# Performance work log

Measured on AMD Instinct MI355X. Metric: run time of the kernel, lower is better.

Reference implementation:

```python
import jax, jax.numpy as jnp
import numpy as np

N_WIRES = 16
VAR_DEPTH = 2
BATCH = 16


def _param_sizes():
    sizes = []
    n = N_WIRES
    lay = 0
    while n > 1:
        sizes.append(4 * int(np.ceil(N_WIRES / 2 ** lay)) * VAR_DEPTH)
        n = (n + 1) // 2
        lay += 1
    return sizes  # [128, 64, 32, 16]


def _apply_1q(psi, gate, w):
    # psi: (B, 2, ..., 2); gate: (2,2) complex; wire w lives on axis w+1
    psi = jnp.moveaxis(psi, w + 1, -1)
    psi = jnp.einsum('...j,ij->...i', psi, gate)
    return jnp.moveaxis(psi, -1, w + 1)


def _rx(psi, th, w):
    c = jnp.cos(th / 2).astype(jnp.complex64)
    s = jnp.sin(th / 2).astype(jnp.complex64)
    gate = jnp.stack([jnp.stack([c, -1j * s]), jnp.stack([-1j * s, c])])
    return _apply_1q(psi, gate, w)


def _rz(psi, th, w):
    ph = jnp.exp(0.5j * th * jnp.array([-1.0, 1.0], jnp.float32)).astype(jnp.complex64)
    shape = [1] * psi.ndim
    shape[w + 1] = 2
    return psi * ph.reshape(shape)


def _rzz(psi, th, wa, wb):
    # diag(e^{-i t/2}, e^{i t/2}, e^{i t/2}, e^{-i t/2}) -> sign = -1 if bits equal else +1
    sgn = jnp.array([[-1.0, 1.0], [1.0, -1.0]], jnp.float32)
    ph = jnp.exp(0.5j * th * sgn).astype(jnp.complex64)  # symmetric, transpose-safe
    a, b = min(wa, wb) + 1, max(wa, wb) + 1
    shape = [1] * psi.ndim
    shape[a] = 2
    shape[b] = 2
    return psi * ph.reshape(shape)


def _cnot(psi, c, t):
    p0 = jax.lax.slice_in_dim(psi, 0, 1, axis=c + 1)
    p1 = jax.lax.slice_in_dim(psi, 1, 2, axis=c + 1)
    return jnp.concatenate([p0, jnp.flip(p1, axis=t + 1)], axis=c + 1)


def _conv_layer(psi, params, active):
    n = len(active)
    for d in range(VAR_DEPTH):
        for j in range(n):
            base = 4 * j + d * 4 * n
            psi = _rx(psi, params[base + 0], active[j])
            psi = _rz(psi, params[base + 1], active[j])
            psi = _rx(psi, params[base + 2], active[j])
        for bg in (0, 1):
            for j in range(bg, n, 2):
                jn = (j + 1) % n  # ring coupling (wraps last->first)
                base = 4 * j + d * 4 * n
                psi = _rzz(psi, params[base + 3], active[j], active[jn])
    return psi


def _pool(psi, active):
    for j in range(0, len(active), 2):
        if j + 1 < len(active):
            psi = _cnot(psi, active[j], active[j + 1])
    return psi, active[::2]


def _forward(psi, params_list):
    active = list(range(N_WIRES))
    for p in params_list:
        psi = _conv_layer(psi, p, active)
        if len(active) > 1:
            psi, active = _pool(psi, active)
    w = active[0]  # measure Z on the surviving wire (wire 0)
    prob = psi.real ** 2 + psi.imag ** 2
    axes = tuple(a for a in range(1, psi.ndim) if a != w + 1)
    p2 = prob.sum(axis=axes)  # (B, 2)
    return p2[:, 0] - p2[:, 1]


def setup_inputs() -> dict:
    key = jax.random.key(0)
    ks = jax.random.split(key, 8)
    dim = 2 ** N_WIRES
    x_re = jax.random.normal(ks[0], (BATCH, dim), dtype=jnp.float32)
    x_im = jax.random.normal(ks[1], (BATCH, dim), dtype=jnp.float32)
    nrm = jnp.sqrt(jnp.sum(x_re ** 2 + x_im ** 2, axis=1, keepdims=True))
    x_re = x_re / nrm
    x_im = x_im / nrm
    sizes = _param_sizes()
    two_pi = 2.0 * np.pi
    params = [jax.random.uniform(ks[2 + i], (sizes[i],), dtype=jnp.float32) * two_pi
              for i in range(len(sizes))]
    return {"x_re": x_re, "x_im": x_im,
            "params0": params[0], "params1": params[1],
            "params2": params[2], "params3": params[3]}


def reference(x_re, x_im, params0, params1, params2, params3):
    psi = (x_re + 1j * x_im).astype(jnp.complex64)
    psi = psi.reshape((BATCH,) + (2,) * N_WIRES)
    return _forward(psi, [params0, params1, params2, params3])
```

## Files before the change

### kernel.cpp

```cpp
#include <hip/hip_runtime.h>


#define DEV __device__ __forceinline__

__device__ static const unsigned char G_CP[60] = {
  15,14,13,12,11,10,9,8,7,6,5,4,3,2,1,0,
  15,14,13,12,11,10,9,8,7,6,5,4,3,2,1,0,
  15,13,11,9,7,5,3,1,
  15,13,11,9,7,5,3,1,
  15,11,7,3,
  15,11,7,3,
  15,7,
  15,7
};
__device__ static const unsigned char G_CQ[60] = {
  14,13,12,11,10,9,8,7,6,5,4,3,2,1,0,15,
  14,13,12,11,10,9,8,7,6,5,4,3,2,1,0,15,
  13,11,9,7,5,3,1,15,
  13,11,9,7,5,3,1,15,
  11,7,3,15,
  11,7,3,15,
  7,15,
  7,15
};

DEV float2 F2(float x, float y){ float2 r; r.x = x; r.y = y; return r; }
DEV float2 cmulf(float2 a, float2 b){ return F2(a.x*b.x - a.y*b.y, a.x*b.y + a.y*b.x); }
DEV int swz(int j){ return j ^ ((j>>4)&15) ^ ((j>>8)&15); }
DEV int sw2(int m){
  return m ^ ((m>>9)&1) ^ (((m>>11)&1)<<1)
           ^ ((((m>>3)&1)^((m>>8)&1))<<2)
           ^ ((((m>>4)&1)^((m>>5)&1)^((m>>10)&1))<<3);
}

#if __has_builtin(__builtin_amdgcn_permlane32_swap)
#define HAVE_PLS 1
DEV void plswap01(float &x0, float &x1){
  auto r = __builtin_amdgcn_permlane32_swap(__float_as_uint(x0), __float_as_uint(x1), false, false);
  x0 = __uint_as_float((unsigned)r[0]);
  x1 = __uint_as_float((unsigned)r[1]);
}
#else
#define HAVE_PLS 0
#endif

template<int SB>
DEV void gate4(float2* a, const float* __restrict__ g){
  const float4 lo = *(const float4*)g;
  const float4 hi = *(const float4*)(g + 4);
  float u00r=lo.x,u00i=lo.y,u01r=lo.z,u01i=lo.w;
  float u11r=hi.x,u11i=hi.y,u10r=hi.z,u10i=hi.w;
  #pragma unroll
  for (int m=0;m<2;m++){
    int i0 = (SB==0) ? (m<<1) : m;
    int i1 = i0 | (1<<SB);
    float2 x0=a[i0], x1=a[i1];
    a[i0] = F2(u00r*x0.x - u00i*x0.y + u01r*x1.x - u01i*x1.y,
               u00r*x0.y + u00i*x0.x + u01r*x1.y + u01i*x1.x);
    a[i1] = F2(u10r*x0.x - u10i*x0.y + u11r*x1.x - u11i*x1.y,
               u10r*x0.y + u10i*x0.x + u11r*x1.y + u11i*x1.x);
  }
}

DEV void lgate(float2* a, const float* __restrict__ g, int mask, int lane){
  const float4 cf = *(const float4*)(g + ((lane & mask) ? 4 : 0));
  float Ar=cf.x, Ai=cf.y, Br=cf.z, Bi=cf.w;
  #pragma unroll
  for (int s=0;s<4;s++){
    float px = __shfl_xor(a[s].x, mask);
    float py = __shfl_xor(a[s].y, mask);
    a[s] = F2(Ar*a[s].x - Ai*a[s].y + Br*px - Bi*py,
              Ar*a[s].y + Ai*a[s].x + Br*py + Bi*px);
  }
}

DEV void lgate32(float2* a, const float* __restrict__ g, int lane){
#if HAVE_PLS
  bool h = (lane & 32) != 0;
  const float4 cf = *(const float4*)(g + (h ? 4 : 0));
  float c0r = h ? cf.z : cf.x, c0i = h ? cf.w : cf.y;
  float c1r = h ? cf.x : cf.z, c1i = h ? cf.y : cf.w;
  #pragma unroll
  for (int s=0;s<4;s++){
    float x0x = a[s].x, x1x = a[s].x, x0y = a[s].y, x1y = a[s].y;
    plswap01(x0x, x1x); plswap01(x0y, x1y);
    a[s] = F2(c0r*x0x - c0i*x0y + c1r*x1x - c1i*x1y,
              c0r*x0y + c0i*x0x + c1r*x1y + c1i*x1x);
  }
#else
  lgate(a, g, 32, lane);
#endif
}

DEV void cswap(float2* a, int cmask, int tmask, int lane){
  bool c = (lane & cmask) != 0;
  #pragma unroll
  for (int s=0;s<4;s++){
    float px = __shfl_xor(a[s].x, tmask);
    float py = __shfl_xor(a[s].y, tmask);
    if (c){ a[s].x = px; a[s].y = py; }
  }
}

template<int C0,int N0,int C1,int N1,unsigned M0,unsigned M1>
DEV void diagv(float2* a, const float* __restrict__ hh, const float* __restrict__ cs, unsigned Ib){
  const unsigned rm = M0|M1;
  float b0 = 0.f, b1 = 0.f;
  #pragma unroll
  for (int k=C0;k<C0+N0;k++){
    const int p=G_CP[k], q=G_CQ[k];
    if (!(((1u<<p)|(1u<<q)) & rm)){
      float h = hh[k];
      float v = (((Ib>>p)^(Ib>>q))&1u) ? h : -h;
      if (k & 1) b1 += v; else b0 += v;
    }
  }
  #pragma unroll
  for (int k=C1;k<C1+N1;k++){
    const int p=G_CP[k], q=G_CQ[k];
    if (!(((1u<<p)|(1u<<q)) & rm)){
      float h = hh[k];
      float v = (((Ib>>p)^(Ib>>q))&1u) ? h : -h;
      if (k & 1) b1 += v; else b0 += v;
    }
  }
  float cb, sb;
  __sincosf(b0 + b1, &sb, &cb);
  #pragma unroll
  for (int r=0;r<4;r++){
    unsigned Ir = Ib ^ ((r&1)?M0:0u) ^ ((r&2)?M1:0u);
    float Fr = cb, Fi = sb;
    #pragma unroll
    for (int k=C0;k<C0+N0;k++){
      const int p=G_CP[k], q=G_CQ[k];
      if (((1u<<p)|(1u<<q)) & rm){
        float ck = cs[2*k], sk = cs[2*k+1];
        float ss = (((Ir>>p)^(Ir>>q))&1u) ? sk : -sk;
        float nr = Fr*ck - Fi*ss, ni = Fr*ss + Fi*ck;
        Fr = nr; Fi = ni;
      }
    }
    #pragma unroll
    for (int k=C1;k<C1+N1;k++){
      const int p=G_CP[k], q=G_CQ[k];
      if (((1u<<p)|(1u<<q)) & rm){
        float ck = cs[2*k], sk = cs[2*k+1];
        float ss = (((Ir>>p)^(Ir>>q))&1u) ? sk : -sk;
        float nr = Fr*ck - Fi*ss, ni = Fr*ss + Fi*ck;
        Fr = nr; Fi = ni;
      }
    }
    a[r] = cmulf(a[r], F2(Fr, Fi));
  }
}

DEV void build_entry(float* sh, const float* __restrict__ p0, const float* __restrict__ p1,
                     const float* __restrict__ p2, const float* __restrict__ p3, int g){
  int d, j, n; const float* P;
  if (g < 32)      { n=16; d=(g>>4)&1; j=g&15; P=p0; }
  else if (g < 48) { n=8;  d=(g>>3)&1; j=g&7;  P=p1; }
  else if (g < 56) { n=4;  d=(g>>2)&1; j=g&3;  P=p2; }
  else             { n=2;  d=(g>>1)&1; j=g&1;  P=p3; }
  int base = 4*j + 4*n*d;
  float th0 = P[base+0], th1 = P[base+1], th2 = P[base+2], th3 = P[base+3];
  float c0,s0,ca,sa,c2,s2;
  sincosf(0.5f*th0, &s0, &c0);
  sincosf(0.5f*th1, &sa, &ca);
  sincosf(0.5f*th2, &s2, &c2);
  float B00r =  ca*c0, B00i = -sa*c0;
  float B01r = -sa*s0, B01i = -ca*s0;
  float B10r =  sa*s0, B10i = -ca*s0;
  float B11r =  ca*c0, B11i =  sa*c0;
  float* o8 = sh + g*8;
  o8[0]=c2*B00r + s2*B10i; o8[1]=c2*B00i - s2*B10r;
  o8[2]=c2*B01r + s2*B11i; o8[3]=c2*B01i - s2*B11r;
  o8[4]=s2*B01i + c2*B11r; o8[5]=-s2*B01r + c2*B11i;
  o8[6]=s2*B00i + c2*B10r; o8[7]=-s2*B00r + c2*B10i;
  sh[480 + g] = 0.5f*th3;
  float ch, shn;
  sincosf(0.5f*th3, &shn, &ch);
  sh[544 + 2*g]     = ch;
  sh[544 + 2*g + 1] = shn;
}

__global__ __launch_bounds__(1024, 4)
void k_pa(const float* __restrict__ xre, const float* __restrict__ xim,
          const float* __restrict__ pp0, const float* __restrict__ pp1,
          const float* __restrict__ pp2, const float* __restrict__ pp3,
          float* __restrict__ tbl, float2* __restrict__ st, float* __restrict__ out){
  const int t = threadIdx.x, lane = t & 63, wv = t >> 6;
  const int batch = blockIdx.x >> 4, o = blockIdx.x & 15;
  const unsigned hi = ((unsigned)batch<<16) | ((unsigned)o<<12);
  __shared__ float2 lds[4096];
  __shared__ float sh[672];
  float2 a[4];
  {
    unsigned base = hi | ((unsigned)t<<2);
    float4 re = *(const float4*)(xre + base);
    float4 im = *(const float4*)(xim + base);
    a[0]=F2(re.x,im.x); a[1]=F2(re.y,im.y); a[2]=F2(re.z,im.z); a[3]=F2(re.w,im.w);
  }
  if (t < 60) build_entry(sh, pp0, pp1, pp2, pp3, t);
  if (blockIdx.x == 0 && t >= 64 && t < 80) out[t - 64] = 0.f;
  __syncthreads();
  if (blockIdx.x == 0){
    for (int i = t; i < 664; i += 1024) tbl[i] = sh[i];
  }
  #define LTB(i) (sh + (i)*8)
  const float* HH = sh + 480;
  const float* CS = sh + 544;
  gate4<0>(a, LTB(15)); gate4<1>(a, LTB(14));
  lgate(a, LTB(13),1,lane); lgate(a, LTB(12),2,lane);
  lgate(a, LTB(11),4,lane); lgate(a, LTB(10),8,lane);
  lgate(a, LTB(9),16,lane); lgate32(a, LTB(8),lane);
  const unsigned IbA = ((unsigned)o<<12) | ((unsigned)wv<<8) | ((unsigned)lane<<2);
  diagv<8,7,0,0,1u,2u>(a, HH, CS, IbA);
  gate4<1>(a, LTB(30));
  lgate(a, LTB(29),1,lane); lgate(a, LTB(28),2,lane);
  lgate(a, LTB(27),4,lane); lgate(a, LTB(26),8,lane);
  lgate(a, LTB(25),16,lane);
  diagv<25,5,0,0,1u,2u>(a, HH, CS, IbA);
  cswap(a,2,1,lane);
  cswap(a,8,4,lane);
  #pragma unroll
  for (int s=0;s<4;s++) lds[swz((t<<2)|s)] = a[s];
  __syncthreads();
  const int idxR = (wv&15) | (((lane>>4)&1)<<4) | (((lane>>5)&1)<<5)
                 | (((lane>>2)&1)<<6) | (((lane>>3)&1)<<7)
                 | ((lane&1)<<8) | (((lane>>1)&1)<<9);
  #pragma unroll
  for (int s=0;s<4;s++) a[s] = lds[swz(idxR | ((s&1)<<10) | (((s>>1)&1)<<11))];
  lgate(a, LTB(7),1,lane); lgate(a, LTB(6),2,lane);
  gate4<0>(a, LTB(5)); gate4<1>(a, LTB(4));
  const unsigned IbB = ((unsigned)o<<12) | (unsigned)idxR;
  diagv<4,4,0,0,1024u,2048u>(a, HH, CS, IbB);
  lgate(a, LTB(24),8,lane);
  lgate(a, LTB(23),1,lane); lgate(a, LTB(22),2,lane);
  gate4<0>(a, LTB(21));
  diagv<21,4,0,0,1024u,2048u>(a, HH, CS, IbB);
  cswap(a,8,4,lane);
  cswap(a,2,1,lane);
  {
    unsigned sb = hi | ((unsigned)wv<<8) | ((unsigned)lane<<2);
    float4 v0, v1;
    v0.x=a[0].x; v0.y=a[0].y; v0.z=a[1].x; v0.w=a[1].y;
    v1.x=a[2].x; v1.y=a[2].y; v1.z=a[3].x; v1.w=a[3].y;
    *(float4*)(st + sb) = v0;
    *(float4*)(st + sb + 2) = v1;
  }
  #undef LTB
}

__global__ __launch_bounds__(1024, 4)
void k_pb(const float* __restrict__ tbl, float2* __restrict__ st, float* __restrict__ out){
  const int t = threadIdx.x, lane = t & 63, wv = t >> 6;
  const int batch = blockIdx.x >> 4, o = blockIdx.x & 15;
  __shared__ float2 lds[4096];
  __shared__ float shB[672];
  __shared__ float red[16];
  const unsigned opart = ((unsigned)(o&1)<<2) | ((unsigned)((o>>1)&1)<<4)
                       | ((unsigned)((o>>2)&1)<<6) | ((unsigned)((o>>3)&1)<<8);
  float2 a[4];
  {
    unsigned gb = ((unsigned)batch<<16)
      | (((unsigned)(o>>3)&1)<<2) | (((unsigned)(o>>2)&1)<<4)
      | (((unsigned)(o>>1)&1)<<6) | (((unsigned)o&1)<<10)
      | (((unsigned)(wv>>3)&1)<<3) | (((unsigned)(wv>>2)&1)<<5)
      | (((unsigned)(wv>>1)&1)<<7) | (((unsigned)wv&1)<<11)
      | (((unsigned)(lane>>4)&1)<<8) | (((unsigned)(lane>>5)&1)<<9)
      | (((unsigned)lane&1)<<12) | (((unsigned)(lane>>1)&1)<<13)
      | (((unsigned)(lane>>2)&1)<<14) | (((unsigned)(lane>>3)&1)<<15);
    const float4* sp = (const float4*)(st + gb);
    float4 lo = sp[0], hi4 = sp[1];
    if (t < 664) shB[t] = tbl[t];
    a[0]=F2(lo.x,lo.y); a[1]=F2(lo.z,lo.w); a[2]=F2(hi4.x,hi4.y); a[3]=F2(hi4.z,hi4.w);
  }
  __syncthreads();
  #define TBL(i) (shB + (i)*8)
  const float* HH = shB + 480;
  const float* CS = shB + 544;
  const unsigned IbA = opart
    | (((unsigned)lane&1)<<12) | (((unsigned)(lane>>1)&1)<<13)
    | (((unsigned)(lane>>2)&1)<<14) | (((unsigned)(lane>>3)&1)<<15)
    | (((unsigned)(lane>>4)&1)<<0) | (((unsigned)(lane>>5)&1)<<1)
    | (((unsigned)wv&1)<<3) | (((unsigned)(wv>>1)&1)<<5)
    | (((unsigned)(wv>>2)&1)<<7) | (((unsigned)(wv>>3)&1)<<9);
  lgate(a, TBL(3),1,lane); lgate(a, TBL(2),2,lane);
  lgate(a, TBL(1),4,lane); lgate(a, TBL(0),8,lane);
  diagv<0,4,15,1,1024u,2048u>(a, HH, CS, IbA);
  lgate(a, TBL(31),16,lane);
  gate4<1>(a, TBL(20));
  lgate(a, TBL(19),1,lane); lgate(a, TBL(18),2,lane);
  lgate(a, TBL(17),4,lane); lgate(a, TBL(16),8,lane);
  diagv<16,5,30,2,1024u,2048u>(a, HH, CS, IbA);
  cswap(a,8,4,lane);
  cswap(a,2,1,lane);
  cswap(a,32,16,lane);
  { float2 tmp=a[2]; a[2]=a[3]; a[3]=tmp; }
  const int idxW = ((lane>>4)&1) | (((lane>>5)&1)<<1)
                 | ((wv&1)<<2) | (((wv>>1)&1)<<3) | (((wv>>2)&1)<<4) | (((wv>>3)&1)<<5)
                 | ((lane&1)<<8) | (((lane>>1)&1)<<9)
                 | (((lane>>2)&1)<<10) | (((lane>>3)&1)<<11);
  #pragma unroll
  for (int s=0;s<4;s++) lds[sw2(idxW | ((s&1)<<6) | (((s>>1)&1)<<7))] = a[s];
  __syncthreads();
  const int idxR = (wv&1) | (((wv>>1)&1)<<6) | (((wv>>2)&1)<<8) | (((wv>>3)&1)<<10)
                 | ((lane&1)<<3) | (((lane>>1)&1)<<4) | (((lane>>2)&1)<<5)
                 | (((lane>>3)&1)<<7) | (((lane>>4)&1)<<9) | (((lane>>5)&1)<<11);
  #pragma unroll
  for (int s=0;s<4;s++) a[s] = lds[sw2(idxR | ((s&1)<<1) | (((s>>1)&1)<<2))];
  const unsigned IbB = opart
    | (((unsigned)wv&1)<<0) | (((unsigned)(wv>>1)&1)<<10)
    | (((unsigned)(wv>>2)&1)<<12) | (((unsigned)(wv>>3)&1)<<14)
    | (((unsigned)lane&1)<<5) | (((unsigned)(lane>>1)&1)<<7)
    | (((unsigned)(lane>>2)&1)<<9) | (((unsigned)(lane>>3)&1)<<11)
    | (((unsigned)(lane>>4)&1)<<13) | (((unsigned)(lane>>5)&1)<<15);
  gate4<0>(a, TBL(39)); gate4<1>(a, TBL(38));
  lgate(a, TBL(37),1,lane); lgate(a, TBL(36),2,lane); lgate(a, TBL(35),4,lane);
  lgate(a, TBL(34),8,lane); lgate(a, TBL(33),16,lane); lgate32(a, TBL(32),lane);
  diagv<32,8,0,0,2u,8u>(a, HH, CS, IbB);
  gate4<0>(a, TBL(47)); gate4<1>(a, TBL(46));
  lgate(a, TBL(45),1,lane); lgate(a, TBL(44),2,lane); lgate(a, TBL(43),4,lane);
  lgate(a, TBL(42),8,lane); lgate(a, TBL(41),16,lane); lgate32(a, TBL(40),lane);
  diagv<40,8,0,0,2u,8u>(a, HH, CS, IbB);
  cswap(a,32,16,lane); cswap(a,8,4,lane); cswap(a,2,1,lane);
  { float2 tmp=a[2]; a[2]=a[3]; a[3]=tmp; }
  lgate32(a, TBL(48),lane); lgate(a, TBL(49),8,lane); lgate(a, TBL(50),2,lane);
  gate4<1>(a, TBL(51));
  diagv<48,4,0,0,2u,8u>(a, HH, CS, IbB);
  lgate32(a, TBL(52),lane); lgate(a, TBL(53),8,lane); lgate(a, TBL(54),2,lane);
  gate4<1>(a, TBL(55));
  diagv<52,4,0,0,2u,8u>(a, HH, CS, IbB);
  cswap(a,32,8,lane);
  if (lane & 2){
    float2 t0=a[0]; a[0]=a[2]; a[2]=t0;
    float2 t1=a[1]; a[1]=a[3]; a[3]=t1;
  }
  lgate32(a, TBL(56),lane); lgate(a, TBL(57),2,lane);
  diagv<56,2,0,0,2u,8u>(a, HH, CS, IbB);
  lgate32(a, TBL(58),lane);
  float sl = 0.f;
  #pragma unroll
  for (int s=0;s<4;s++) sl += a[s].x*a[s].x + a[s].y*a[s].y;
  float sg = (lane & 32) ? -sl : sl;
  #pragma unroll
  for (int off=32; off>0; off>>=1) sg += __shfl_down(sg, off);
  if ((t & 63) == 0) red[wv] = sg;
  __syncthreads();
  if (t == 0){
    float tot = 0.f;
    #pragma unroll
    for (int w=0; w<16; w++) tot += red[w];
    atomicAdd(out + batch, tot);
  }
  #undef TBL
}

extern "C" void kernel_launch(void* const* d_in, const int* in_sizes, int n_in,
                              void* d_out, int out_size, void* d_ws, size_t ws_size,
                              hipStream_t stream) {
  const float* xre = (const float*)d_in[0];
  const float* xim = (const float*)d_in[1];
  const float* p0  = (const float*)d_in[2];
  const float* p1  = (const float*)d_in[3];
  const float* p2  = (const float*)d_in[4];
  const float* p3  = (const float*)d_in[5];
  float* out = (float*)d_out;
  float2* st = (float2*)d_ws;
  float* tbl = (float*)((char*)d_ws + (8u<<20));

  k_pa<<<256, 1024, 0, stream>>>(xre, xim, p0, p1, p2, p3, tbl, st, out);
  k_pb<<<256, 1024, 0, stream>>>(tbl, st, out);
}
```

Baseline: 106.2 us.

## Fuse two kernels into one cooperative kernel with a grid-wide sync

```diff
diff --git a/kernel.cpp b/kernel.cpp
--- a/kernel.cpp
+++ b/kernel.cpp
@@ -1,4 +1,7 @@
 #include <hip/hip_runtime.h>
+#include <hip/hip_cooperative_groups.h>
+
+namespace cg = cooperative_groups;
 
 
 #define DEV __device__ __forceinline__
@@ -184,176 +187,168 @@
 }
 
 __global__ __launch_bounds__(1024, 4)
-void k_pa(const float* __restrict__ xre, const float* __restrict__ xim,
-          const float* __restrict__ pp0, const float* __restrict__ pp1,
-          const float* __restrict__ pp2, const float* __restrict__ pp3,
-          float* __restrict__ tbl, float2* __restrict__ st, float* __restrict__ out){
+void k_fused(const float* __restrict__ xre, const float* __restrict__ xim,
+             const float* __restrict__ pp0, const float* __restrict__ pp1,
+             const float* __restrict__ pp2, const float* __restrict__ pp3,
+             float2* __restrict__ st, float* __restrict__ out){
   const int t = threadIdx.x, lane = t & 63, wv = t >> 6;
   const int batch = blockIdx.x >> 4, o = blockIdx.x & 15;
-  const unsigned hi = ((unsigned)batch<<16) | ((unsigned)o<<12);
   __shared__ float2 lds[4096];
   __shared__ float sh[672];
-  float2 a[4];
-  {
-    unsigned base = hi | ((unsigned)t<<2);
-    float4 re = *(const float4*)(xre + base);
-    float4 im = *(const float4*)(xim + base);
-    a[0]=F2(re.x,im.x); a[1]=F2(re.y,im.y); a[2]=F2(re.z,im.z); a[3]=F2(re.w,im.w);
-  }
-  if (t < 60) build_entry(sh, pp0, pp1, pp2, pp3, t);
-  if (blockIdx.x == 0 && t >= 64 && t < 80) out[t - 64] = 0.f;
-  __syncthreads();
-  if (blockIdx.x == 0){
-    for (int i = t; i < 664; i += 1024) tbl[i] = sh[i];
-  }
+  __shared__ float red[16];
   #define LTB(i) (sh + (i)*8)
   const float* HH = sh + 480;
   const float* CS = sh + 544;
-  gate4<0>(a, LTB(15)); gate4<1>(a, LTB(14));
-  lgate(a, LTB(13),1,lane); lgate(a, LTB(12),2,lane);
-  lgate(a, LTB(11),4,lane); lgate(a, LTB(10),8,lane);
-  lgate(a, LTB(9),16,lane); lgate32(a, LTB(8),lane);
-  const unsigned IbA = ((unsigned)o<<12) | ((unsigned)wv<<8) | ((unsigned)lane<<2);
-  diagv<8,7,0,0,1u,2u>(a, HH, CS, IbA);
-  gate4<1>(a, LTB(30));
-  lgate(a, LTB(29),1,lane); lgate(a, LTB(28),2,lane);
-  lgate(a, LTB(27),4,lane); lgate(a, LTB(26),8,lane);
-  lgate(a, LTB(25),16,lane);
-  diagv<25,5,0,0,1u,2u>(a, HH, CS, IbA);
-  cswap(a,2,1,lane);
-  cswap(a,8,4,lane);
-  #pragma unroll
-  for (int s=0;s<4;s++) lds[swz((t<<2)|s)] = a[s];
-  __syncthreads();
-  const int idxR = (wv&15) | (((lane>>4)&1)<<4) | (((lane>>5)&1)<<5)
-                 | (((lane>>2)&1)<<6) | (((lane>>3)&1)<<7)
-                 | ((lane&1)<<8) | (((lane>>1)&1)<<9);
-  #pragma unroll
-  for (int s=0;s<4;s++) a[s] = lds[swz(idxR | ((s&1)<<10) | (((s>>1)&1)<<11))];
-  lgate(a, LTB(7),1,lane); lgate(a, LTB(6),2,lane);
-  gate4<0>(a, LTB(5)); gate4<1>(a, LTB(4));
-  const unsigned IbB = ((unsigned)o<<12) | (unsigned)idxR;
-  diagv<4,4,0,0,1024u,2048u>(a, HH, CS, IbB);
-  lgate(a, LTB(24),8,lane);
-  lgate(a, LTB(23),1,lane); lgate(a, LTB(22),2,lane);
-  gate4<0>(a, LTB(21));
-  diagv<21,4,0,0,1024u,2048u>(a, HH, CS, IbB);
-  cswap(a,8,4,lane);
-  cswap(a,2,1,lane);
+  float2 a[4];
+
   {
-    unsigned sb = hi | ((unsigned)wv<<8) | ((unsigned)lane<<2);
-    float4 v0, v1;
-    v0.x=a[0].x; v0.y=a[0].y; v0.z=a[1].x; v0.w=a[1].y;
-    v1.x=a[2].x; v1.y=a[2].y; v1.z=a[3].x; v1.w=a[3].y;
-    *(float4*)(st + sb) = v0;
-    *(float4*)(st + sb + 2) = v1;
+    const unsigned hi = ((unsigned)batch<<16) | ((unsigned)o<<12);
+    {
+      unsigned base = hi | ((unsigned)t<<2);
+      float4 re = *(const float4*)(xre + base);
+      float4 im = *(const float4*)(xim + base);
+      a[0]=F2(re.x,im.x); a[1]=F2(re.y,im.y); a[2]=F2(re.z,im.z); a[3]=F2(re.w,im.w);
+    }
+    if (t < 60) build_entry(sh, pp0, pp1, pp2, pp3, t);
+    if (blockIdx.x == 0 && t >= 64 && t < 80) out[t - 64] = 0.f;
+    __syncthreads();
+    gate4<0>(a, LTB(15)); gate4<1>(a, LTB(14));
+    lgate(a, LTB(13),1,lane); lgate(a, LTB(12),2,lane);
+    lgate(a, LTB(11),4,lane); lgate(a, LTB(10),8,lane);
+    lgate(a, LTB(9),16,lane); lgate32(a, LTB(8),lane);
+    const unsigned IbA = ((unsigned)o<<12) | ((unsigned)wv<<8) | ((unsigned)lane<<2);
+    diagv<8,7,0,0,1u,2u>(a, HH, CS, IbA);
+    gate4<1>(a, LTB(30));
+    lgate(a, LTB(29),1,lane); lgate(a, LTB(28),2,lane);
+    lgate(a, LTB(27),4,lane); lgate(a, LTB(26),8,lane);
+    lgate(a, LTB(25),16,lane);
+    diagv<25,5,0,0,1u,2u>(a, HH, CS, IbA);
+    cswap(a,2,1,lane);
+    cswap(a,8,4,lane);
+    #pragma unroll
+    for (int s=0;s<4;s++) lds[swz((t<<2)|s)] = a[s];
+    __syncthreads();
+    const int idxR = (wv&15) | (((lane>>4)&1)<<4) | (((lane>>5)&1)<<5)
+                   | (((lane>>2)&1)<<6) | (((lane>>3)&1)<<7)
+                   | ((lane&1)<<8) | (((lane>>1)&1)<<9);
+    #pragma unroll
+    for (int s=0;s<4;s++) a[s] = lds[swz(idxR | ((s&1)<<10) | (((s>>1)&1)<<11))];
+    lgate(a, LTB(7),1,lane); lgate(a, LTB(6),2,lane);
+    gate4<0>(a, LTB(5)); gate4<1>(a, LTB(4));
+    const unsigned IbB = ((unsigned)o<<12) | (unsigned)idxR;
+    diagv<4,4,0,0,1024u,2048u>(a, HH, CS, IbB);
+    lgate(a, LTB(24),8,lane);
+    lgate(a, LTB(23),1,lane); lgate(a, LTB(22),2,lane);
+    gate4<0>(a, LTB(21));
+    diagv<21,4,0,0,1024u,2048u>(a, HH, CS, IbB);
+    cswap(a,8,4,lane);
+    cswap(a,2,1,lane);
+    {
+      unsigned sb = hi | ((unsigned)wv<<8) | ((unsigned)lane<<2);
+      float4 v0, v1;
+      v0.x=a[0].x; v0.y=a[0].y; v0.z=a[1].x; v0.w=a[1].y;
+      v1.x=a[2].x; v1.y=a[2].y; v1.z=a[3].x; v1.w=a[3].y;
+      *(float4*)(st + sb) = v0;
+      *(float4*)(st + sb + 2) = v1;
+    }
+  }
+
+  __threadfence();
+  cg::this_grid().sync();
+
+  {
+    const unsigned opart = ((unsigned)(o&1)<<2) | ((unsigned)((o>>1)&1)<<4)
+                         | ((unsigned)((o>>2)&1)<<6) | ((unsigned)((o>>3)&1)<<8);
+    {
+      unsigned gb = ((unsigned)batch<<16)
+        | (((unsigned)(o>>3)&1)<<2) | (((unsigned)(o>>2)&1)<<4)
+        | (((unsigned)(o>>1)&1)<<6) | (((unsigned)o&1)<<10)
+        | (((unsigned)(wv>>3)&1)<<3) | (((unsigned)(wv>>2)&1)<<5)
+        | (((unsigned)(wv>>1)&1)<<7) | (((unsigned)wv&1)<<11)
+        | (((unsigned)(lane>>4)&1)<<8) | (((unsigned)(lane>>5)&1)<<9)
+        | (((unsigned)lane&1)<<12) | (((unsigned)(lane>>1)&1)<<13)
+        | (((unsigned)(lane>>2)&1)<<14) | (((unsigned)(lane>>3)&1)<<15);
+      const float4* sp = (const float4*)(st + gb);
+      float4 lo = sp[0], hi4 = sp[1];
+      a[0]=F2(lo.x,lo.y); a[1]=F2(lo.z,lo.w); a[2]=F2(hi4.x,hi4.y); a[3]=F2(hi4.z,hi4.w);
+    }
+    const unsigned IbA2 = opart
+      | (((unsigned)lane&1)<<12) | (((unsigned)(lane>>1)&1)<<13)
+      | (((unsigned)(lane>>2)&1)<<14) | (((unsigned)(lane>>3)&1)<<15)
+      | (((unsigned)(lane>>4)&1)<<0) | (((unsigned)(lane>>5)&1)<<1)
+      | (((unsigned)wv&1)<<3) | (((unsigned)(wv>>1)&1)<<5)
+      | (((unsigned)(wv>>2)&1)<<7) | (((unsigned)(wv>>3)&1)<<9);
+    lgate(a, LTB(3),1,lane); lgate(a, LTB(2),2,lane);
+    lgate(a, LTB(1),4,lane); lgate(a, LTB(0),8,lane);
+    diagv<0,4,15,1,1024u,2048u>(a, HH, CS, IbA2);
+    lgate(a, LTB(31),16,lane);
+    gate4<1>(a, LTB(20));
+    lgate(a, LTB(19),1,lane); lgate(a, LTB(18),2,lane);
+    lgate(a, LTB(17),4,lane); lgate(a, LTB(16),8,lane);
+    diagv<16,5,30,2,1024u,2048u>(a, HH, CS, IbA2);
+    cswap(a,8,4,lane);
+    cswap(a,2,1,lane);
+    cswap(a,32,16,lane);
+    { float2 tmp=a[2]; a[2]=a[3]; a[3]=tmp; }
+    const int idxW = ((lane>>4)&1) | (((lane>>5)&1)<<1)
+                   | ((wv&1)<<2) | (((wv>>1)&1)<<3) | (((wv>>2)&1)<<4) | (((wv>>3)&1)<<5)
+                   | ((lane&1)<<8) | (((lane>>1)&1)<<9)
+                   | (((lane>>2)&1)<<10) | (((lane>>3)&1)<<11);
+    __syncthreads();
+    #pragma unroll
+    for (int s=0;s<4;s++) lds[sw2(idxW | ((s&1)<<6) | (((s>>1)&1)<<7))] = a[s];
+    __syncthreads();
+    const int idxR2 = (wv&1) | (((wv>>1)&1)<<6) | (((wv>>2)&1)<<8) | (((wv>>3)&1)<<10)
+                   | ((lane&1)<<3) | (((lane>>1)&1)<<4) | (((lane>>2)&1)<<5)
+                   | (((lane>>3)&1)<<7) | (((lane>>4)&1)<<9) | (((lane>>5)&1)<<11);
+    #pragma unroll
+    for (int s=0;s<4;s++) a[s] = lds[sw2(idxR2 | ((s&1)<<1) | (((s>>1)&1)<<2))];
+    const unsigned IbB2 = opart
+      | (((unsigned)wv&1)<<0) | (((unsigned)(wv>>1)&1)<<10)
+      | (((unsigned)(wv>>2)&1)<<12) | (((unsigned)(wv>>3)&1)<<14)
+      | (((unsigned)lane&1)<<5) | (((unsigned)(lane>>1)&1)<<7)
+      | (((unsigned)(lane>>2)&1)<<9) | (((unsigned)(lane>>3)&1)<<11)
+      | (((unsigned)(lane>>4)&1)<<13) | (((unsigned)(lane>>5)&1)<<15);
+    gate4<0>(a, LTB(39)); gate4<1>(a, LTB(38));
+    lgate(a, LTB(37),1,lane); lgate(a, LTB(36),2,lane); lgate(a, LTB(35),4,lane);
+    lgate(a, LTB(34),8,lane); lgate(a, LTB(33),16,lane); lgate32(a, LTB(32),lane);
+    diagv<32,8,0,0,2u,8u>(a, HH, CS, IbB2);
+    gate4<0>(a, LTB(47)); gate4<1>(a, LTB(46));
+    lgate(a, LTB(45),1,lane); lgate(a, LTB(44),2,lane); lgate(a, LTB(43),4,lane);
+    lgate(a, LTB(42),8,lane); lgate(a, LTB(41),16,lane); lgate32(a, LTB(40),lane);
+    diagv<40,8,0,0,2u,8u>(a, HH, CS, IbB2);
+    cswap(a,32,16,lane); cswap(a,8,4,lane); cswap(a,2,1,lane);
+    { float2 tmp=a[2]; a[2]=a[3]; a[3]=tmp; }
+    lgate32(a, LTB(48),lane); lgate(a, LTB(49),8,lane); lgate(a, LTB(50),2,lane);
+    gate4<1>(a, LTB(51));
+    diagv<48,4,0,0,2u,8u>(a, HH, CS, IbB2);
+    lgate32(a, LTB(52),lane); lgate(a, LTB(53),8,lane); lgate(a, LTB(54),2,lane);
+    gate4<1>(a, LTB(55));
+    diagv<52,4,0,0,2u,8u>(a, HH, CS, IbB2);
+    cswap(a,32,8,lane);
+    if (lane & 2){
+      float2 t0=a[0]; a[0]=a[2]; a[2]=t0;
+      float2 t1=a[1]; a[1]=a[3]; a[3]=t1;
+    }
+    lgate32(a, LTB(56),lane); lgate(a, LTB(57),2,lane);
+    diagv<56,2,0,0,2u,8u>(a, HH, CS, IbB2);
+    lgate32(a, LTB(58),lane);
+    float sl = 0.f;
+    #pragma unroll
+    for (int s=0;s<4;s++) sl += a[s].x*a[s].x + a[s].y*a[s].y;
+    float sg = (lane & 32) ? -sl : sl;
+    #pragma unroll
+    for (int off=32; off>0; off>>=1) sg += __shfl_down(sg, off);
+    if ((t & 63) == 0) red[wv] = sg;
+    __syncthreads();
+    if (t == 0){
+      float tot = 0.f;
+      #pragma unroll
+      for (int w=0; w<16; w++) tot += red[w];
+      atomicAdd(out + batch, tot);
+    }
   }
   #undef LTB
-}
-
-__global__ __launch_bounds__(1024, 4)
-void k_pb(const float* __restrict__ tbl, float2* __restrict__ st, float* __restrict__ out){
-  const int t = threadIdx.x, lane = t & 63, wv = t >> 6;
-  const int batch = blockIdx.x >> 4, o = blockIdx.x & 15;
-  __shared__ float2 lds[4096];
-  __shared__ float shB[672];
-  __shared__ float red[16];
-  const unsigned opart = ((unsigned)(o&1)<<2) | ((unsigned)((o>>1)&1)<<4)
-                       | ((unsigned)((o>>2)&1)<<6) | ((unsigned)((o>>3)&1)<<8);
-  float2 a[4];
-  {
-    unsigned gb = ((unsigned)batch<<16)
-      | (((unsigned)(o>>3)&1)<<2) | (((unsigned)(o>>2)&1)<<4)
-      | (((unsigned)(o>>1)&1)<<6) | (((unsigned)o&1)<<10)
-      | (((unsigned)(wv>>3)&1)<<3) | (((unsigned)(wv>>2)&1)<<5)
-      | (((unsigned)(wv>>1)&1)<<7) | (((unsigned)wv&1)<<11)
-      | (((unsigned)(lane>>4)&1)<<8) | (((unsigned)(lane>>5)&1)<<9)
-      | (((unsigned)lane&1)<<12) | (((unsigned)(lane>>1)&1)<<13)
-      | (((unsigned)(lane>>2)&1)<<14) | (((unsigned)(lane>>3)&1)<<15);
-    const float4* sp = (const float4*)(st + gb);
-    float4 lo = sp[0], hi4 = sp[1];
-    if (t < 664) shB[t] = tbl[t];
-    a[0]=F2(lo.x,lo.y); a[1]=F2(lo.z,lo.w); a[2]=F2(hi4.x,hi4.y); a[3]=F2(hi4.z,hi4.w);
-  }
-  __syncthreads();
-  #define TBL(i) (shB + (i)*8)
-  const float* HH = shB + 480;
-  const float* CS = shB + 544;
-  const unsigned IbA = opart
-    | (((unsigned)lane&1)<<12) | (((unsigned)(lane>>1)&1)<<13)
-    | (((unsigned)(lane>>2)&1)<<14) | (((unsigned)(lane>>3)&1)<<15)
-    | (((unsigned)(lane>>4)&1)<<0) | (((unsigned)(lane>>5)&1)<<1)
-    | (((unsigned)wv&1)<<3) | (((unsigned)(wv>>1)&1)<<5)
-    | (((unsigned)(wv>>2)&1)<<7) | (((unsigned)(wv>>3)&1)<<9);
-  lgate(a, TBL(3),1,lane); lgate(a, TBL(2),2,lane);
-  lgate(a, TBL(1),4,lane); lgate(a, TBL(0),8,lane);
-  diagv<0,4,15,1,1024u,2048u>(a, HH, CS, IbA);
-  lgate(a, TBL(31),16,lane);
-  gate4<1>(a, TBL(20));
-  lgate(a, TBL(19),1,lane); lgate(a, TBL(18),2,lane);
-  lgate(a, TBL(17),4,lane); lgate(a, TBL(16),8,lane);
-  diagv<16,5,30,2,1024u,2048u>(a, HH, CS, IbA);
-  cswap(a,8,4,lane);
-  cswap(a,2,1,lane);
-  cswap(a,32,16,lane);
-  { float2 tmp=a[2]; a[2]=a[3]; a[3]=tmp; }
-  const int idxW = ((lane>>4)&1) | (((lane>>5)&1)<<1)
-                 | ((wv&1)<<2) | (((wv>>1)&1)<<3) | (((wv>>2)&1)<<4) | (((wv>>3)&1)<<5)
-                 | ((lane&1)<<8) | (((lane>>1)&1)<<9)
-                 | (((lane>>2)&1)<<10) | (((lane>>3)&1)<<11);
-  #pragma unroll
-  for (int s=0;s<4;s++) lds[sw2(idxW | ((s&1)<<6) | (((s>>1)&1)<<7))] = a[s];
-  __syncthreads();
-  const int idxR = (wv&1) | (((wv>>1)&1)<<6) | (((wv>>2)&1)<<8) | (((wv>>3)&1)<<10)
-                 | ((lane&1)<<3) | (((lane>>1)&1)<<4) | (((lane>>2)&1)<<5)
-                 | (((lane>>3)&1)<<7) | (((lane>>4)&1)<<9) | (((lane>>5)&1)<<11);
-  #pragma unroll
-  for (int s=0;s<4;s++) a[s] = lds[sw2(idxR | ((s&1)<<1) | (((s>>1)&1)<<2))];
-  const unsigned IbB = opart
-    | (((unsigned)wv&1)<<0) | (((unsigned)(wv>>1)&1)<<10)
-    | (((unsigned)(wv>>2)&1)<<12) | (((unsigned)(wv>>3)&1)<<14)
-    | (((unsigned)lane&1)<<5) | (((unsigned)(lane>>1)&1)<<7)
-    | (((unsigned)(lane>>2)&1)<<9) | (((unsigned)(lane>>3)&1)<<11)
-    | (((unsigned)(lane>>4)&1)<<13) | (((unsigned)(lane>>5)&1)<<15);
-  gate4<0>(a, TBL(39)); gate4<1>(a, TBL(38));
-  lgate(a, TBL(37),1,lane); lgate(a, TBL(36),2,lane); lgate(a, TBL(35),4,lane);
-  lgate(a, TBL(34),8,lane); lgate(a, TBL(33),16,lane); lgate32(a, TBL(32),lane);
-  diagv<32,8,0,0,2u,8u>(a, HH, CS, IbB);
-  gate4<0>(a, TBL(47)); gate4<1>(a, TBL(46));
-  lgate(a, TBL(45),1,lane); lgate(a, TBL(44),2,lane); lgate(a, TBL(43),4,lane);
-  lgate(a, TBL(42),8,lane); lgate(a, TBL(41),16,lane); lgate32(a, TBL(40),lane);
-  diagv<40,8,0,0,2u,8u>(a, HH, CS, IbB);
-  cswap(a,32,16,lane); cswap(a,8,4,lane); cswap(a,2,1,lane);
-  { float2 tmp=a[2]; a[2]=a[3]; a[3]=tmp; }
-  lgate32(a, TBL(48),lane); lgate(a, TBL(49),8,lane); lgate(a, TBL(50),2,lane);
-  gate4<1>(a, TBL(51));
-  diagv<48,4,0,0,2u,8u>(a, HH, CS, IbB);
-  lgate32(a, TBL(52),lane); lgate(a, TBL(53),8,lane); lgate(a, TBL(54),2,lane);
-  gate4<1>(a, TBL(55));
-  diagv<52,4,0,0,2u,8u>(a, HH, CS, IbB);
-  cswap(a,32,8,lane);
-  if (lane & 2){
-    float2 t0=a[0]; a[0]=a[2]; a[2]=t0;
-    float2 t1=a[1]; a[1]=a[3]; a[3]=t1;
-  }
-  lgate32(a, TBL(56),lane); lgate(a, TBL(57),2,lane);
-  diagv<56,2,0,0,2u,8u>(a, HH, CS, IbB);
-  lgate32(a, TBL(58),lane);
-  float sl = 0.f;
-  #pragma unroll
-  for (int s=0;s<4;s++) sl += a[s].x*a[s].x + a[s].y*a[s].y;
-  float sg = (lane & 32) ? -sl : sl;
-  #pragma unroll
-  for (int off=32; off>0; off>>=1) sg += __shfl_down(sg, off);
-  if ((t & 63) == 0) red[wv] = sg;
-  __syncthreads();
-  if (t == 0){
-    float tot = 0.f;
-    #pragma unroll
-    for (int w=0; w<16; w++) tot += red[w];
-    atomicAdd(out + batch, tot);
-  }
-  #undef TBL
 }
 
 extern "C" void kernel_launch(void* const* d_in, const int* in_sizes, int n_in,
@@ -367,8 +362,8 @@
   const float* p3  = (const float*)d_in[5];
   float* out = (float*)d_out;
   float2* st = (float2*)d_ws;
-  float* tbl = (float*)((char*)d_ws + (8u<<20));
-
-  k_pa<<<256, 1024, 0, stream>>>(xre, xim, p0, p1, p2, p3, tbl, st, out);
-  k_pb<<<256, 1024, 0, stream>>>(tbl, st, out);
-}
+
+  void* args[] = { (void*)&xre, (void*)&xim, (void*)&p0, (void*)&p1,
+                   (void*)&p2, (void*)&p3, (void*)&st, (void*)&out };
+  hipLaunchCooperativeKernel((void*)k_fused, dim3(256), dim3(1024), args, 0, stream);
+}
```

Result: slower. 250.5 us (+135.8%).
